# Kernel optimization log

Measured on AMD Instinct MI355X. Metric: run time of the kernel, lower is better.

Reference implementation:

```python
import jax, jax.numpy as jnp
import numpy as np

H = 16  # num_heads
ROPE_BASE = 10000.0

def _rotate_half(x):
    d = x.shape[-1]
    return jnp.concatenate((-x[..., d // 2:], x[..., :d // 2]), axis=-1)

def setup_inputs() -> dict:
    key = jax.random.key(0)
    ks = jax.random.split(key, 9)
    B, S, E = 4, 2048, 1024
    s = 0.02
    return {
        "x": jax.random.normal(ks[0], (B, S, E), dtype=jnp.float32),
        "wq": jax.random.normal(ks[1], (E, E), dtype=jnp.float32) * s,
        "bq": jax.random.normal(ks[2], (E,), dtype=jnp.float32) * s,
        "wk": jax.random.normal(ks[3], (E, E), dtype=jnp.float32) * s,
        "bk": jax.random.normal(ks[4], (E,), dtype=jnp.float32) * s,
        "wv": jax.random.normal(ks[5], (E, E), dtype=jnp.float32) * s,
        "bv": jax.random.normal(ks[6], (E,), dtype=jnp.float32) * s,
        "wo": jax.random.normal(ks[7], (E, E), dtype=jnp.float32) * s,
        "bo": jax.random.normal(ks[8], (E,), dtype=jnp.float32) * s,
    }

def reference(x, wq, bq, wk, bk, wv, bv, wo, bo):
    B, S, E = x.shape
    D = E // H  # head_dim
    # projections (nn.Linear: x @ W.T + b), then split heads -> (B, H, S, D)
    def proj(w, b):
        return (x @ w.T + b).reshape(B, S, H, D).transpose(0, 2, 1, 3)
    q = proj(wq, bq)
    k = proj(wk, bk)
    v = proj(wv, bv)
    # RoPE: freqs (S, D//2) -> repeat_interleave(2) -> (S, D)
    inv_freq = 1.0 / (ROPE_BASE ** (jnp.arange(0, D, 2, dtype=jnp.float32) / D))
    freqs = jnp.arange(S, dtype=jnp.float32)[:, None] * inv_freq[None, :]
    cos = jnp.repeat(jnp.cos(freqs), 2, axis=-1)[None, None]  # (1,1,S,D)
    sin = jnp.repeat(jnp.sin(freqs), 2, axis=-1)[None, None]
    q = q * cos + _rotate_half(q) * sin
    k = k * cos + _rotate_half(k) * sin
    scale = D ** (-0.5)
    scores = jnp.einsum('bhqd,bhkd->bhqk', q, k) * scale
    attn = jax.nn.softmax(scores, axis=-1)
    out = jnp.einsum('bhqk,bhkd->bhqd', attn, v)  # (B,H,S,D)
    out = out.transpose(0, 2, 1, 3).reshape(B, S, E)
    return out @ wo.T + bo
```

## Files before the change

kernel.cpp:

```cpp
#include <hip/hip_runtime.h>


typedef __attribute__((ext_vector_type(4))) float f32x4;
typedef __attribute__((ext_vector_type(16))) float f32x16;
typedef __attribute__((ext_vector_type(8))) short bfrag;
typedef __attribute__((ext_vector_type(4))) short svec4;
typedef __attribute__((ext_vector_type(4))) unsigned u32x4;

#define MFMA16(a, b, c) __builtin_amdgcn_mfma_f32_16x16x32_bf16(a, b, c, 0, 0, 0)
#define MFMA32(a, b, c) __builtin_amdgcn_mfma_f32_32x32x16_bf16(a, b, c, 0, 0, 0)

__device__ __forceinline__ unsigned short f2bf(float f) {
  unsigned u = __builtin_bit_cast(unsigned, f);
  u += 0x7FFFu + ((u >> 16) & 1u);
  return (unsigned short)(u >> 16);
}

__device__ __forceinline__ void gload16(const void* g, void* l) {
  __builtin_amdgcn_global_load_lds(
      (const __attribute__((address_space(1))) unsigned int*)g,
      (__attribute__((address_space(3))) unsigned int*)l, 16, 0, 0);
}

__global__ __launch_bounds__(256) void prep_kernel(
    const float* __restrict__ x, const float* __restrict__ wq,
    const float* __restrict__ wk, const float* __restrict__ wv,
    const float* __restrict__ wo,
    unsigned short* __restrict__ xb, unsigned short* __restrict__ wqb,
    unsigned short* __restrict__ wkb, unsigned short* __restrict__ wvb,
    unsigned short* __restrict__ wob, float2* __restrict__ rope) {
  const int y = blockIdx.y;
  const int tid = blockIdx.x * blockDim.x + threadIdx.x;
  const int stride = gridDim.x * blockDim.x;
  if (y < 5) {
    const float* src = y == 0 ? x : y == 1 ? wq : y == 2 ? wk : y == 3 ? wv : wo;
    unsigned short* dst = y == 0 ? xb : y == 1 ? wqb : y == 2 ? wkb : y == 3 ? wvb : wob;
    const int n4 = (y == 0 ? (8192 * 1024) : (1024 * 1024)) >> 2;
    for (int i = tid; i < n4; i += stride) {
      float4 v = ((const float4*)src)[i];
      svec4 o;
      o.x = (short)f2bf(v.x); o.y = (short)f2bf(v.y);
      o.z = (short)f2bf(v.z); o.w = (short)f2bf(v.w);
      ((svec4*)dst)[i] = o;
    }
  } else {
    for (int i = tid; i < 2048 * 32; i += stride) {
      int s = i >> 5, f = i & 31;
      float invf = powf(10000.0f, -(float)f * (1.0f / 32.0f));
      float ang = (float)s * invf;
      rope[i] = make_float2(cosf(ang), sinf(ang));
    }
  }
}

__global__ __launch_bounds__(256) void gemm_qkv(
    const unsigned short* __restrict__ Xb,
    const unsigned short* __restrict__ Wq, const unsigned short* __restrict__ Wk,
    const unsigned short* __restrict__ Wv,
    const float* __restrict__ biasq, const float* __restrict__ biask,
    const float* __restrict__ biasv,
    const float2* __restrict__ rope,
    unsigned short* __restrict__ Qo, unsigned short* __restrict__ Ko,
    unsigned short* __restrict__ Vto) {
  const int bid = blockIdx.x;
  const int xg = bid / 192;
  const int j  = bid % 192;
  const int yb = j % 64;
  const int z  = j / 64;
  __shared__ unsigned short As[128 * 64];
  __shared__ unsigned short Bs[128 * 64];
  const int t = threadIdx.x;
  const int lane = t & 63, w = t >> 6;
  const int wr = w >> 1, wc = w & 1;
  const int lc = lane & 15, lr = lane >> 4;

  int m0, n0;
  const unsigned short *Apt, *Bpt;
  if (z == 0)      { m0 = yb * 128; n0 = xg * 128; Apt = Xb; Bpt = Wq; }
  else if (z == 1) { m0 = yb * 128; n0 = xg * 128; Apt = Xb; Bpt = Wk; }
  else             { m0 = xg * 128; n0 = yb * 128; Apt = Wv; Bpt = Xb; }

  const int arow = t >> 3;
  const int acol = ((t & 7) << 3) ^ ((arow & 7) << 3);
  const unsigned short* gA = Apt + (size_t)(m0 + arow) * 1024 + acol;
  const unsigned short* gB = Bpt + (size_t)(n0 + arow) * 1024 + acol;
  unsigned short* lA = As + t * 8;
  unsigned short* lB = Bs + t * 8;

  f32x4 acc[4][4];
#pragma unroll
  for (int m = 0; m < 4; ++m)
#pragma unroll
    for (int n = 0; n < 4; ++n) acc[m][n] = (f32x4){0.f, 0.f, 0.f, 0.f};

  const int rsw = (lc & 7) << 3;

#pragma unroll 1
  for (int kt = 0; kt < 16; ++kt) {
    __syncthreads();
#pragma unroll
    for (int c = 0; c < 4; ++c) {
      gload16(gA + (size_t)c * 32 * 1024, lA + c * 2048);
      gload16(gB + (size_t)c * 32 * 1024, lB + c * 2048);
    }
    gA += 64; gB += 64;
    __syncthreads();
#pragma unroll
    for (int ks = 0; ks < 2; ++ks) {
      bfrag af[4], bfr[4];
#pragma unroll
      for (int i = 0; i < 4; ++i)
        af[i] = *(const bfrag*)(As + (wr * 64 + i * 16 + lc) * 64 + ((ks * 32 + lr * 8) ^ rsw));
#pragma unroll
      for (int i = 0; i < 4; ++i)
        bfr[i] = *(const bfrag*)(Bs + (wc * 64 + i * 16 + lc) * 64 + ((ks * 32 + lr * 8) ^ rsw));
#pragma unroll
      for (int m = 0; m < 4; ++m)
#pragma unroll
        for (int n = 0; n < 4; ++n)
          acc[m][n] = MFMA16(af[m], bfr[n], acc[m][n]);
    }
  }

  if (z < 2) {
    const float* bias = (z == 0) ? biasq : biask;
    unsigned short* dst = (z == 0) ? Qo : Ko;
    const float qs = (z == 0) ? 0.125f * 1.44269504f : 1.0f;
    const int h = (n0 + wc * 64) >> 6;
#pragma unroll
    for (int m = 0; m < 4; ++m) {
#pragma unroll
      for (int r = 0; r < 4; ++r) {
        int row = m0 + wr * 64 + m * 16 + lr * 4 + r;
        int b = row >> 11, s = row & 2047;
        const float2* trow = rope + (s << 5);
        size_t base = ((size_t)((b << 4) + h) * 2048 + s) * 64;
#pragma unroll
        for (int n = 0; n < 2; ++n) {
          int col1 = n0 + wc * 64 + n * 16 + lc;
          int d = n * 16 + lc;
          float a  = acc[m][n][r]     + bias[col1];
          float bb = acc[m][n + 2][r] + bias[col1 + 32];
          float2 t0 = trow[d >> 1];
          float2 t1 = trow[16 + (d >> 1)];
          dst[base + d]      = f2bf((a * t0.x - bb * t0.y) * qs);
          dst[base + d + 32] = f2bf((bb * t1.x + a * t1.y) * qs);
        }
      }
    }
  } else {
#pragma unroll
    for (int m = 0; m < 4; ++m) {
#pragma unroll
      for (int r = 0; r < 4; ++r) {
        int wcol = m0 + wr * 64 + m * 16 + lr * 4 + r;
        float bv = biasv[wcol];
        int h = wcol >> 6, d = wcol & 63;
#pragma unroll
        for (int n = 0; n < 4; ++n) {
          int token = n0 + wc * 64 + n * 16 + lc;
          int b = token >> 11, s = token & 2047;
          Vto[((size_t)((b << 4) + h) * 64 + d) * 2048 + s] = f2bf(acc[m][n][r] + bv);
        }
      }
    }
  }
}

__global__ __launch_bounds__(256) void attn_kernel(
    const unsigned short* __restrict__ Q, const unsigned short* __restrict__ K,
    const unsigned short* __restrict__ Vt, unsigned short* __restrict__ O) {
  __shared__ unsigned short Ks[2][64 * 64];
  __shared__ unsigned short Vs[2][64 * 64];
  const int t = threadIdx.x;
  const int lane = t & 63, w = t >> 6;
  const int l31 = lane & 31, th = lane >> 5;
  const int bid = blockIdx.x;
  const int xcd = bid & 7;
  const int jj = bid >> 3;
  const int bh = xcd * 8 + (jj >> 3);
  const int qb = jj & 7;
  const int q0 = qb * 256 + w * 64;

  const unsigned short* Qp = Q + ((size_t)bh * 2048 + q0 + l31) * 64 + th * 8;
  bfrag bq0[4], bq1[4];
#pragma unroll
  for (int kk = 0; kk < 4; ++kk) {
    bq0[kk] = *(const bfrag*)(Qp + kk * 16);
    bq1[kk] = *(const bfrag*)(Qp + 32 * 64 + kk * 16);
  }

  f32x16 acc00, acc01, acc10, acc11;
#pragma unroll
  for (int i = 0; i < 16; ++i) {
    acc00[i] = 0.f; acc01[i] = 0.f; acc10[i] = 0.f; acc11[i] = 0.f;
  }
  float lsum0 = 0.f, lsum1 = 0.f;

  const unsigned short* Kg = K + (size_t)bh * 2048 * 64;
  const unsigned short* Vg = Vt + (size_t)bh * 64 * 2048;

  const int rs = (l31 & 7) << 3;

  const int srow = t >> 3;
  const int scol = ((t & 7) ^ (srow & 7)) << 3;

#define STAGE(bufi, kb_)                                                        \
  {                                                                             \
    gload16(Kg + (size_t)((kb_) + srow) * 64 + scol,        Ks[bufi] + t * 8);  \
    gload16(Kg + (size_t)((kb_) + 32 + srow) * 64 + scol,   Ks[bufi] + 2048 + t * 8); \
    gload16(Vg + (size_t)srow * 2048 + (kb_) + scol,        Vs[bufi] + t * 8);  \
    gload16(Vg + (size_t)(32 + srow) * 2048 + (kb_) + scol, Vs[bufi] + 2048 + t * 8); \
  }

  STAGE(0, 0);
  STAGE(1, 64);
  int cur = 0;

#pragma unroll 1
  for (int kt = 0; kt < 32; ++kt) {
    if (kt < 30) { asm volatile("s_waitcnt vmcnt(4)" ::: "memory"); }
    else         { asm volatile("s_waitcnt vmcnt(0)" ::: "memory"); }
    __builtin_amdgcn_s_barrier();

    const unsigned short* KsC = Ks[cur];
    const unsigned short* VsC = Vs[cur];

    bfrag pa0[4], pa1[4];

#pragma unroll
    for (int kb = 0; kb < 2; ++kb) {
      const unsigned short* kp = KsC + (kb * 32 + l31) * 64;
      bfrag ka[4];
#pragma unroll
      for (int kk = 0; kk < 4; ++kk)
        ka[kk] = *(const bfrag*)(kp + ((kk * 16 + th * 8) ^ rs));

#pragma unroll
      for (int g = 0; g < 2; ++g) {
        f32x16 sc;
#pragma unroll
        for (int i = 0; i < 16; ++i) sc[i] = 0.f;
        __builtin_amdgcn_s_setprio(1);
#pragma unroll
        for (int kk = 0; kk < 4; ++kk)
          sc = MFMA32(ka[kk], g == 0 ? bq0[kk] : bq1[kk], sc);
        __builtin_amdgcn_s_setprio(0);

#pragma unroll
        for (int i = 0; i < 16; ++i) sc[i] = __builtin_amdgcn_exp2f(sc[i]);
        {
          float s0 = (sc[0] + sc[1]) + (sc[2] + sc[3]);
          float s1 = (sc[4] + sc[5]) + (sc[6] + sc[7]);
          float s2 = (sc[8] + sc[9]) + (sc[10] + sc[11]);
          float s3 = (sc[12] + sc[13]) + (sc[14] + sc[15]);
          if (g == 0) lsum0 += (s0 + s1) + (s2 + s3);
          else        lsum1 += (s0 + s1) + (s2 + s3);
        }

        unsigned pk[4][2];
#pragma unroll
        for (int gg = 0; gg < 4; ++gg) {
          asm("v_cvt_pk_bf16_f32 %0, %1, %2"
              : "=v"(pk[gg][0]) : "v"(sc[4 * gg]), "v"(sc[4 * gg + 1]));
          asm("v_cvt_pk_bf16_f32 %0, %1, %2"
              : "=v"(pk[gg][1]) : "v"(sc[4 * gg + 2]), "v"(sc[4 * gg + 3]));
        }
#pragma unroll
        for (int ka2 = 0; ka2 < 2; ++ka2) {
          u32x4 pu;
#pragma unroll
          for (int j = 0; j < 2; ++j) {
            unsigned zlo = pk[2 * ka2][j];
            unsigned zhi = pk[2 * ka2 + 1][j];
            unsigned zsend = th ? zlo : zhi;
            unsigned wv = (unsigned)__shfl_xor((int)zsend, 32);
            pu[j]     = th ? wv : zlo;
            pu[2 + j] = th ? zhi : wv;
          }
          if (g == 0) pa0[kb * 2 + ka2] = __builtin_bit_cast(bfrag, pu);
          else        pa1[kb * 2 + ka2] = __builtin_bit_cast(bfrag, pu);
        }
      }
    }

    __builtin_amdgcn_s_setprio(1);
#pragma unroll
    for (int kg = 0; kg < 4; ++kg) {
      const unsigned short* vp0 = VsC + (size_t)l31 * 64;
      const unsigned short* vp1 = VsC + (size_t)(32 + l31) * 64;
      bfrag vb0 = *(const bfrag*)(vp0 + ((kg * 16 + th * 8) ^ rs));
      bfrag vb1 = *(const bfrag*)(vp1 + ((kg * 16 + th * 8) ^ rs));
      acc00 = MFMA32(pa0[kg], vb0, acc00);
      acc01 = MFMA32(pa0[kg], vb1, acc01);
      acc10 = MFMA32(pa1[kg], vb0, acc10);
      acc11 = MFMA32(pa1[kg], vb1, acc11);
    }
    __builtin_amdgcn_s_setprio(0);

    __builtin_amdgcn_s_barrier();
    if (kt + 2 < 32) STAGE(cur, (kt + 2) * 64);
    cur ^= 1;
  }
#undef STAGE

  float v0 = lsum0 + __shfl_xor(lsum0, 32);
  float v1 = lsum1 + __shfl_xor(lsum1, 32);
  float inv0 = 1.0f / v0;
  float inv1 = 1.0f / v1;

  const int b = bh >> 4, h = bh & 15;
#pragma unroll
  for (int r = 0; r < 16; ++r) {
    int qrow = (r & 3) + 8 * (r >> 2) + 4 * th;
    float invr0 = __shfl(inv0, qrow);
    float invr1 = __shfl(inv1, qrow);
    size_t base0 = (((size_t)b * 2048 + q0 + qrow) * 16 + h) * 64 + l31;
    size_t base1 = (((size_t)b * 2048 + q0 + 32 + qrow) * 16 + h) * 64 + l31;
    O[base0]      = f2bf(acc00[r] * invr0);
    O[base0 + 32] = f2bf(acc01[r] * invr0);
    O[base1]      = f2bf(acc10[r] * invr1);
    O[base1 + 32] = f2bf(acc11[r] * invr1);
  }
}

__global__ __launch_bounds__(256) void gemm_out(
    const unsigned short* __restrict__ Ob, const unsigned short* __restrict__ Wo,
    const float* __restrict__ bias, float* __restrict__ out) {
  __shared__ unsigned short As[128 * 64];
  __shared__ unsigned short Bs[128 * 64];
  const int bid = blockIdx.x;
  const int xg = bid / 64;
  const int j  = bid % 64;
  const int t = threadIdx.x;
  const int lane = t & 63, w = t >> 6;
  const int wr = w >> 1, wc = w & 1;
  const int lc = lane & 15, lr = lane >> 4;
  const int m0 = j * 128, n0 = xg * 128;

  const int arow = t >> 3;
  const int acol = ((t & 7) << 3) ^ ((arow & 7) << 3);
  const unsigned short* gA = Ob + (size_t)(m0 + arow) * 1024 + acol;
  const unsigned short* gB = Wo + (size_t)(n0 + arow) * 1024 + acol;
  unsigned short* lA = As + t * 8;
  unsigned short* lB = Bs + t * 8;

  f32x4 acc[4][4];
#pragma unroll
  for (int m = 0; m < 4; ++m)
#pragma unroll
    for (int n = 0; n < 4; ++n) acc[m][n] = (f32x4){0.f, 0.f, 0.f, 0.f};

  const int rsw = (lc & 7) << 3;

#pragma unroll 1
  for (int kt = 0; kt < 16; ++kt) {
    __syncthreads();
#pragma unroll
    for (int c = 0; c < 4; ++c) {
      gload16(gA + (size_t)c * 32 * 1024, lA + c * 2048);
      gload16(gB + (size_t)c * 32 * 1024, lB + c * 2048);
    }
    gA += 64; gB += 64;
    __syncthreads();
#pragma unroll
    for (int ks = 0; ks < 2; ++ks) {
      bfrag af[4], bfr[4];
#pragma unroll
      for (int i = 0; i < 4; ++i)
        af[i] = *(const bfrag*)(As + (wr * 64 + i * 16 + lc) * 64 + ((ks * 32 + lr * 8) ^ rsw));
#pragma unroll
      for (int i = 0; i < 4; ++i)
        bfr[i] = *(const bfrag*)(Bs + (wc * 64 + i * 16 + lc) * 64 + ((ks * 32 + lr * 8) ^ rsw));
#pragma unroll
      for (int m = 0; m < 4; ++m)
#pragma unroll
        for (int n = 0; n < 4; ++n)
          acc[m][n] = MFMA16(af[m], bfr[n], acc[m][n]);
    }
  }
#pragma unroll
  for (int n = 0; n < 4; ++n) {
    int col = n0 + wc * 64 + n * 16 + lc;
    float bv = bias[col];
#pragma unroll
    for (int m = 0; m < 4; ++m) {
#pragma unroll
      for (int r = 0; r < 4; ++r) {
        int row = m0 + wr * 64 + m * 16 + lr * 4 + r;
        out[(size_t)row * 1024 + col] = acc[m][n][r] + bv;
      }
    }
  }
}

extern "C" void kernel_launch(void* const* d_in, const int* in_sizes, int n_in,
                              void* d_out, int out_size, void* d_ws, size_t ws_size,
                              hipStream_t stream) {
  (void)in_sizes; (void)n_in; (void)out_size; (void)ws_size;
  const float* x  = (const float*)d_in[0];
  const float* wq = (const float*)d_in[1];
  const float* bq = (const float*)d_in[2];
  const float* wk = (const float*)d_in[3];
  const float* bk = (const float*)d_in[4];
  const float* wv = (const float*)d_in[5];
  const float* bv = (const float*)d_in[6];
  const float* wo = (const float*)d_in[7];
  const float* bo = (const float*)d_in[8];
  float* out = (float*)d_out;

  char* ws = (char*)d_ws;
  unsigned short* Xb   = (unsigned short*)(ws);
  unsigned short* Wqb  = (unsigned short*)(ws + (16ull << 20));
  unsigned short* Wkb  = (unsigned short*)(ws + (18ull << 20));
  unsigned short* Wvb  = (unsigned short*)(ws + (20ull << 20));
  unsigned short* Wob  = (unsigned short*)(ws + (22ull << 20));
  unsigned short* Qb   = (unsigned short*)(ws + (24ull << 20));
  unsigned short* Kb   = (unsigned short*)(ws + (40ull << 20));
  unsigned short* Vt   = (unsigned short*)(ws + (56ull << 20));
  float2* rope         = (float2*)(ws + (72ull << 20));
  unsigned short* Ob   = Xb;

  prep_kernel<<<dim3(1024, 6), 256, 0, stream>>>(x, wq, wk, wv, wo,
                                                 Xb, Wqb, Wkb, Wvb, Wob, rope);
  gemm_qkv<<<1536, 256, 0, stream>>>(Xb, Wqb, Wkb, Wvb,
                                     bq, bk, bv, rope, Qb, Kb, Vt);
  attn_kernel<<<512, 256, 0, stream>>>(Qb, Kb, Vt, Ob);
  gemm_out<<<512, 256, 0, stream>>>(Ob, Wob, bo, out);
}
```

Before: 195.3 us.

## Software-pipeline attention loop so PV MFMAs overlap exp of next score block

Restructures the attention inner loop into two half-steps. The PV MFMAs for the previously exponentiated probability block are interleaved with the QK^T MFMAs of the current half, and the exp/pack of each half runs after its MFMAs. This lets transcendental and VALU work overlap matrix-core work instead of serialising per tile. The last half-block's PV product is carried across the loop barrier in registers (with its V fragments preloaded) and flushed after the loop. The cost is higher register pressure and more complex code.

```diff
diff --git a/kernel.cpp b/kernel.cpp
--- a/kernel.cpp
+++ b/kernel.cpp
@@ -20,6 +20,41 @@
   __builtin_amdgcn_global_load_lds(
       (const __attribute__((address_space(1))) unsigned int*)g,
       (__attribute__((address_space(3))) unsigned int*)l, 16, 0, 0);
+}
+
+__device__ __forceinline__ void exppack(f32x16& sc, float& ls, int th,
+                                        bfrag& paA, bfrag& paB) {
+#pragma unroll
+  for (int i = 0; i < 16; ++i) sc[i] = __builtin_amdgcn_exp2f(sc[i]);
+  ls += ((sc[0] + sc[1]) + (sc[2] + sc[3])) + ((sc[4] + sc[5]) + (sc[6] + sc[7])) +
+        ((sc[8] + sc[9]) + (sc[10] + sc[11])) + ((sc[12] + sc[13]) + (sc[14] + sc[15]));
+  unsigned pk[4][2];
+#pragma unroll
+  for (int gg = 0; gg < 4; ++gg) {
+    asm("v_cvt_pk_bf16_f32 %0, %1, %2"
+        : "=v"(pk[gg][0]) : "v"(sc[4 * gg]), "v"(sc[4 * gg + 1]));
+    asm("v_cvt_pk_bf16_f32 %0, %1, %2"
+        : "=v"(pk[gg][1]) : "v"(sc[4 * gg + 2]), "v"(sc[4 * gg + 3]));
+  }
+  u32x4 puA, puB;
+#pragma unroll
+  for (int j = 0; j < 2; ++j) {
+    unsigned zlo = pk[0][j], zhi = pk[1][j];
+    unsigned zsend = th ? zlo : zhi;
+    unsigned wv = (unsigned)__shfl_xor((int)zsend, 32);
+    puA[j]     = th ? wv : zlo;
+    puA[2 + j] = th ? zhi : wv;
+  }
+#pragma unroll
+  for (int j = 0; j < 2; ++j) {
+    unsigned zlo = pk[2][j], zhi = pk[3][j];
+    unsigned zsend = th ? zlo : zhi;
+    unsigned wv = (unsigned)__shfl_xor((int)zsend, 32);
+    puB[j]     = th ? wv : zlo;
+    puB[2 + j] = th ? zhi : wv;
+  }
+  paA = __builtin_bit_cast(bfrag, puA);
+  paB = __builtin_bit_cast(bfrag, puB);
 }
 
 __global__ __launch_bounds__(256) void prep_kernel(
@@ -217,6 +252,10 @@
   STAGE(1, 64);
   int cur = 0;
 
+  const bfrag zf = (bfrag){0, 0, 0, 0, 0, 0, 0, 0};
+  bfrag paP0 = zf, paP1 = zf, paP2 = zf, paP3 = zf;
+  bfrag vbP00 = zf, vbP01 = zf, vbP10 = zf, vbP11 = zf;
+
 #pragma unroll 1
   for (int kt = 0; kt < 32; ++kt) {
     if (kt < 30) { asm volatile("s_waitcnt vmcnt(4)" ::: "memory"); }
@@ -226,83 +265,76 @@
     const unsigned short* KsC = Ks[cur];
     const unsigned short* VsC = Vs[cur];
 
-    bfrag pa0[4], pa1[4];
-
-#pragma unroll
-    for (int kb = 0; kb < 2; ++kb) {
-      const unsigned short* kp = KsC + (kb * 32 + l31) * 64;
-      bfrag ka[4];
-#pragma unroll
-      for (int kk = 0; kk < 4; ++kk)
-        ka[kk] = *(const bfrag*)(kp + ((kk * 16 + th * 8) ^ rs));
-
-#pragma unroll
-      for (int g = 0; g < 2; ++g) {
-        f32x16 sc;
-#pragma unroll
-        for (int i = 0; i < 16; ++i) sc[i] = 0.f;
-        __builtin_amdgcn_s_setprio(1);
-#pragma unroll
-        for (int kk = 0; kk < 4; ++kk)
-          sc = MFMA32(ka[kk], g == 0 ? bq0[kk] : bq1[kk], sc);
-        __builtin_amdgcn_s_setprio(0);
-
-#pragma unroll
-        for (int i = 0; i < 16; ++i) sc[i] = __builtin_amdgcn_exp2f(sc[i]);
-        {
-          float s0 = (sc[0] + sc[1]) + (sc[2] + sc[3]);
-          float s1 = (sc[4] + sc[5]) + (sc[6] + sc[7]);
-          float s2 = (sc[8] + sc[9]) + (sc[10] + sc[11]);
-          float s3 = (sc[12] + sc[13]) + (sc[14] + sc[15]);
-          if (g == 0) lsum0 += (s0 + s1) + (s2 + s3);
-          else        lsum1 += (s0 + s1) + (s2 + s3);
-        }
-
-        unsigned pk[4][2];
-#pragma unroll
-        for (int gg = 0; gg < 4; ++gg) {
-          asm("v_cvt_pk_bf16_f32 %0, %1, %2"
-              : "=v"(pk[gg][0]) : "v"(sc[4 * gg]), "v"(sc[4 * gg + 1]));
-          asm("v_cvt_pk_bf16_f32 %0, %1, %2"
-              : "=v"(pk[gg][1]) : "v"(sc[4 * gg + 2]), "v"(sc[4 * gg + 3]));
-        }
-#pragma unroll
-        for (int ka2 = 0; ka2 < 2; ++ka2) {
-          u32x4 pu;
-#pragma unroll
-          for (int j = 0; j < 2; ++j) {
-            unsigned zlo = pk[2 * ka2][j];
-            unsigned zhi = pk[2 * ka2 + 1][j];
-            unsigned zsend = th ? zlo : zhi;
-            unsigned wv = (unsigned)__shfl_xor((int)zsend, 32);
-            pu[j]     = th ? wv : zlo;
-            pu[2 + j] = th ? zhi : wv;
-          }
-          if (g == 0) pa0[kb * 2 + ka2] = __builtin_bit_cast(bfrag, pu);
-          else        pa1[kb * 2 + ka2] = __builtin_bit_cast(bfrag, pu);
-        }
-      }
-    }
-
+    bfrag ka[4];
+#pragma unroll
+    for (int kk = 0; kk < 4; ++kk)
+      ka[kk] = *(const bfrag*)(KsC + l31 * 64 + ((kk * 16 + th * 8) ^ rs));
+    f32x16 sc0, sc1;
+#pragma unroll
+    for (int i = 0; i < 16; ++i) { sc0[i] = 0.f; sc1[i] = 0.f; }
     __builtin_amdgcn_s_setprio(1);
 #pragma unroll
-    for (int kg = 0; kg < 4; ++kg) {
-      const unsigned short* vp0 = VsC + (size_t)l31 * 64;
-      const unsigned short* vp1 = VsC + (size_t)(32 + l31) * 64;
-      bfrag vb0 = *(const bfrag*)(vp0 + ((kg * 16 + th * 8) ^ rs));
-      bfrag vb1 = *(const bfrag*)(vp1 + ((kg * 16 + th * 8) ^ rs));
-      acc00 = MFMA32(pa0[kg], vb0, acc00);
-      acc01 = MFMA32(pa0[kg], vb1, acc01);
-      acc10 = MFMA32(pa1[kg], vb0, acc10);
-      acc11 = MFMA32(pa1[kg], vb1, acc11);
-    }
+    for (int kk = 0; kk < 4; ++kk) sc0 = MFMA32(ka[kk], bq0[kk], sc0);
+#pragma unroll
+    for (int kk = 0; kk < 4; ++kk) sc1 = MFMA32(ka[kk], bq1[kk], sc1);
+    acc00 = MFMA32(paP0, vbP00, acc00);
+    acc01 = MFMA32(paP0, vbP01, acc01);
+    acc10 = MFMA32(paP2, vbP00, acc10);
+    acc11 = MFMA32(paP2, vbP01, acc11);
+    acc00 = MFMA32(paP1, vbP10, acc00);
+    acc01 = MFMA32(paP1, vbP11, acc01);
+    acc10 = MFMA32(paP3, vbP10, acc10);
+    acc11 = MFMA32(paP3, vbP11, acc11);
     __builtin_amdgcn_s_setprio(0);
+    bfrag paA0, paA1, paA2, paA3;
+    exppack(sc0, lsum0, th, paA0, paA1);
+    exppack(sc1, lsum1, th, paA2, paA3);
+
+#pragma unroll
+    for (int kk = 0; kk < 4; ++kk)
+      ka[kk] = *(const bfrag*)(KsC + (32 + l31) * 64 + ((kk * 16 + th * 8) ^ rs));
+    f32x16 sd0, sd1;
+#pragma unroll
+    for (int i = 0; i < 16; ++i) { sd0[i] = 0.f; sd1[i] = 0.f; }
+    bfrag vb00 = *(const bfrag*)(VsC + (size_t)l31 * 64        + ((0 * 16 + th * 8) ^ rs));
+    bfrag vb01 = *(const bfrag*)(VsC + (size_t)(32 + l31) * 64 + ((0 * 16 + th * 8) ^ rs));
+    bfrag vb10 = *(const bfrag*)(VsC + (size_t)l31 * 64        + ((1 * 16 + th * 8) ^ rs));
+    bfrag vb11 = *(const bfrag*)(VsC + (size_t)(32 + l31) * 64 + ((1 * 16 + th * 8) ^ rs));
+    __builtin_amdgcn_s_setprio(1);
+#pragma unroll
+    for (int kk = 0; kk < 4; ++kk) sd0 = MFMA32(ka[kk], bq0[kk], sd0);
+#pragma unroll
+    for (int kk = 0; kk < 4; ++kk) sd1 = MFMA32(ka[kk], bq1[kk], sd1);
+    acc00 = MFMA32(paA0, vb00, acc00);
+    acc01 = MFMA32(paA0, vb01, acc01);
+    acc10 = MFMA32(paA2, vb00, acc10);
+    acc11 = MFMA32(paA2, vb01, acc11);
+    acc00 = MFMA32(paA1, vb10, acc00);
+    acc01 = MFMA32(paA1, vb11, acc01);
+    acc10 = MFMA32(paA3, vb10, acc10);
+    acc11 = MFMA32(paA3, vb11, acc11);
+    __builtin_amdgcn_s_setprio(0);
+    exppack(sd0, lsum0, th, paP0, paP1);
+    exppack(sd1, lsum1, th, paP2, paP3);
+    vbP00 = *(const bfrag*)(VsC + (size_t)l31 * 64        + ((2 * 16 + th * 8) ^ rs));
+    vbP01 = *(const bfrag*)(VsC + (size_t)(32 + l31) * 64 + ((2 * 16 + th * 8) ^ rs));
+    vbP10 = *(const bfrag*)(VsC + (size_t)l31 * 64        + ((3 * 16 + th * 8) ^ rs));
+    vbP11 = *(const bfrag*)(VsC + (size_t)(32 + l31) * 64 + ((3 * 16 + th * 8) ^ rs));
 
     __builtin_amdgcn_s_barrier();
     if (kt + 2 < 32) STAGE(cur, (kt + 2) * 64);
     cur ^= 1;
   }
 #undef STAGE
+
+  acc00 = MFMA32(paP0, vbP00, acc00);
+  acc01 = MFMA32(paP0, vbP01, acc01);
+  acc10 = MFMA32(paP2, vbP00, acc10);
+  acc11 = MFMA32(paP2, vbP01, acc11);
+  acc00 = MFMA32(paP1, vbP10, acc00);
+  acc01 = MFMA32(paP1, vbP11, acc01);
+  acc10 = MFMA32(paP3, vbP10, acc10);
+  acc11 = MFMA32(paP3, vbP11, acc11);
 
   float v0 = lsum0 + __shfl_xor(lsum0, 32);
   float v1 = lsum1 + __shfl_xor(lsum1, 32);
```

Measured after the change: 223.6 us. 1.14x slower.
